# Optimization experiments

Hardware: AMD Instinct MI355X
Metric: run time of the kernel (lower is better)

Reference implementation:

```python
import jax, jax.numpy as jnp
import numpy as np

B, T, P = 4, 512, 3584          # batch, new tokens per seq, cached tokens per seq
D_MODEL, H, KH, DH = 2048, 16, 4, 128
N_REP = H // KH
MAX_SEQ = 4096
ROPE_BASE = 1e6
EPS = 1e-6


def _rmsnorm(t, w):
    # t: [..., DH]
    var = jnp.mean(t * t, axis=-1, keepdims=True)
    return t * jax.lax.rsqrt(var + EPS) * w


def _rope(t, positions):
    # t: [N, heads, DH], positions: [N] int
    half = DH // 2
    inv_freq = (1.0 / ROPE_BASE) ** (2.0 * jnp.arange(half, dtype=jnp.float32) / DH)
    theta = positions.astype(jnp.float32)[:, None] * inv_freq[None, :]   # [N, half]
    theta = jnp.concatenate([theta, theta], axis=-1)                      # [N, DH]
    sin = jnp.sin(theta)[:, None, :]
    cos = jnp.cos(theta)[:, None, :]
    x1, x2 = jnp.split(t, 2, axis=-1)
    rot = jnp.concatenate([-x2, x1], axis=-1)
    return cos * t + sin * rot


def setup_inputs() -> dict:
    key = jax.random.key(0)
    ks = jax.random.split(key, 9)
    N = B * T
    x = jax.random.normal(ks[0], (N, D_MODEL), dtype=jnp.float32)
    k_cache = jax.random.normal(ks[1], (B, KH, P, DH), dtype=jnp.float32)
    v_cache = jax.random.normal(ks[2], (B, KH, P, DH), dtype=jnp.float32)
    s = 1.0 / np.sqrt(D_MODEL)
    w_q = jax.random.normal(ks[3], (H * DH, D_MODEL), dtype=jnp.float32) * s
    w_k = jax.random.normal(ks[4], (KH * DH, D_MODEL), dtype=jnp.float32) * s
    w_v = jax.random.normal(ks[5], (KH * DH, D_MODEL), dtype=jnp.float32) * s
    w_o = jax.random.normal(ks[6], (D_MODEL, H * DH), dtype=jnp.float32) * s
    q_norm_w = jnp.ones((DH,), dtype=jnp.float32)
    k_norm_w = jnp.ones((DH,), dtype=jnp.float32)
    # each sequence's new tokens occupy absolute positions [P, P+T)
    positions = jnp.tile(P + jnp.arange(T, dtype=jnp.int32), B)  # [B*T]
    return {"x": x, "k_cache": k_cache, "v_cache": v_cache,
            "w_q": w_q, "w_k": w_k, "w_v": w_v, "w_o": w_o,
            "q_norm_w": q_norm_w, "k_norm_w": k_norm_w,
            "positions": positions}


def reference(x, k_cache, v_cache, w_q, w_k, w_v, w_o, q_norm_w, k_norm_w, positions):
    N = x.shape[0]
    # QKV projections (no bias)
    q = (x @ w_q.T).reshape(N, H, DH)
    k = (x @ w_k.T).reshape(N, KH, DH)
    v = (x @ w_v.T).reshape(N, KH, DH)
    # per-head RMSNorm then RoPE at absolute positions
    q = _rope(_rmsnorm(q, q_norm_w), positions)
    k = _rope(_rmsnorm(k, k_norm_w), positions)
    # assemble full KV: cached (pre-rotated) past + new tokens
    k_new = k.reshape(B, T, KH, DH).transpose(0, 2, 1, 3)   # [B,KH,T,DH]
    v_new = v.reshape(B, T, KH, DH).transpose(0, 2, 1, 3)
    k_full = jnp.concatenate([k_cache, k_new], axis=2)       # [B,KH,P+T,DH]
    v_full = jnp.concatenate([v_cache, v_new], axis=2)
    # GQA: repeat each kv head n_rep times
    k_rep = jnp.repeat(k_full, N_REP, axis=1)                # [B,H,S,DH]
    v_rep = jnp.repeat(v_full, N_REP, axis=1)
    q4 = q.reshape(B, T, H, DH).transpose(0, 2, 1, 3)        # [B,H,T,DH]
    scale = 1.0 / jnp.sqrt(jnp.float32(DH))
    scores = jnp.einsum('bhtd,bhsd->bhts', q4, k_rep) * scale  # [B,H,T,P+T]
    # right-bottom causal mask: q_pos = P + t, kv_pos = s
    q_pos = P + jnp.arange(T)
    kv_pos = jnp.arange(P + T)
    mask = q_pos[:, None] >= kv_pos[None, :]
    scores = jnp.where(mask[None, None], scores, -jnp.inf)
    attn = jax.nn.softmax(scores, axis=-1)
    out = jnp.einsum('bhts,bhsd->bhtd', attn, v_rep)          # [B,H,T,DH]
    out = out.transpose(0, 2, 1, 3).reshape(N, H * DH)
    return out @ w_o.T
```

## Files before the change

kernel.cpp:

```cpp
#include <hip/hip_runtime.h>
#include <hip/hip_bf16.h>
#include <stdint.h>

#define B_   4
#define T_   512
#define P_   3584
#define S_   4096
#define H_   16
#define KH_  4
#define DM_  2048
#define DH_  128
#define NTOK 2048
#define NCHUNK 3
#define NROWS 32768

typedef __attribute__((ext_vector_type(8)))  short          bf16x8;
typedef __attribute__((ext_vector_type(4)))  float          f32x4;
typedef __attribute__((ext_vector_type(16))) float          f32x16;
typedef __attribute__((ext_vector_type(4)))  float          f4v;
typedef __attribute__((ext_vector_type(4)))  unsigned short us4v;

__device__ __forceinline__ unsigned short f2bf(float x) {
    union { float f; unsigned u; } v; v.f = x;
    unsigned r = v.u + 0x7FFFu + ((v.u >> 16) & 1u);
    return (unsigned short)(r >> 16);
}
__device__ __forceinline__ float bf2f(unsigned short b) {
    union { unsigned u; float f; } v; v.u = ((unsigned)b) << 16; return v.f;
}
__device__ __forceinline__ unsigned pkbf(float a, float b) {
    __hip_bfloat162 h = __float22bfloat162_rn(float2{a, b});
    union { __hip_bfloat162 h; unsigned u; } cv; cv.h = h; return cv.u;
}
__device__ __forceinline__ float ex2(float x) {
    float r; asm("v_exp_f32 %0, %1" : "=v"(r) : "v"(x)); return r;
}
__device__ __forceinline__ float max3f(float a, float b, float c) {
    float r; asm("v_max3_f32 %0, %1, %2, %3" : "=v"(r) : "v"(a), "v"(b), "v"(c)); return r;
}
__device__ __forceinline__ float sin_rev(float xf) {
    float r; asm("v_sin_f32 %0, %1" : "=v"(r) : "v"(xf)); return r;
}
__device__ __forceinline__ float cos_rev(float xf) {
    float r; asm("v_cos_f32 %0, %1" : "=v"(r) : "v"(xf)); return r;
}

#define GLDS16(gp, lp) __builtin_amdgcn_global_load_lds( \
    (const __attribute__((address_space(1))) void*)(gp), \
    (__attribute__((address_space(3))) void*)(lp), 16, 0, 0)

__global__ __launch_bounds__(256) void convert_all(
    const float* __restrict__ x,  const float* __restrict__ wq,
    const float* __restrict__ wk, const float* __restrict__ wv,
    const float* __restrict__ wo, const float* __restrict__ kc,
    const float* __restrict__ vc,
    unsigned short* __restrict__ xb,   unsigned short* __restrict__ wqkvb,
    unsigned short* __restrict__ wob,  unsigned short* __restrict__ kfull,
    unsigned short* __restrict__ vT)
{
    __shared__ unsigned short tile[64][65];
    if (blockIdx.x >= 2048) {
        const int id = blockIdx.x - 2048;
        const int bk = id / 112;
        const int rem = id % 112;
        const int st = rem >> 1;
        const int dt = rem & 1;
        const float* src = vc + ((size_t)bk * P_ + st * 64) * DH_ + dt * 64;
        const int tq = threadIdx.x & 15;
        const int ts = threadIdx.x >> 4;
        #pragma unroll
        for (int i = 0; i < 4; ++i) {
            const int si = ts + i * 16;
            f4v v = *(const f4v*)(src + (size_t)si * DH_ + tq * 4);
            tile[si][tq*4+0] = f2bf(v[0]); tile[si][tq*4+1] = f2bf(v[1]);
            tile[si][tq*4+2] = f2bf(v[2]); tile[si][tq*4+3] = f2bf(v[3]);
        }
        __syncthreads();
        unsigned short* dst = vT + ((size_t)bk * DH_ + dt * 64) * S_ + st * 64;
        const int sq = threadIdx.x & 15;
        const int td = threadIdx.x >> 4;
        #pragma unroll
        for (int i = 0; i < 4; ++i) {
            const int di = td + i * 16;
            us4v o;
            o[0] = tile[sq*4+0][di]; o[1] = tile[sq*4+1][di];
            o[2] = tile[sq*4+2][di]; o[3] = tile[sq*4+3][di];
            *(us4v*)(dst + (size_t)di * S_ + sq * 4) = o;
        }
        return;
    }
    const long total = 5505024;
    for (long i = (long)blockIdx.x * 256 + threadIdx.x; i < total;
         i += 2048L * 256) {
        const f4v* src; us4v* dst; long s4, d4;
        if (i < 1048576)      { src=(const f4v*)x;  dst=(us4v*)xb;              s4=i;         d4=s4; }
        else if (i < 2097152) { src=(const f4v*)wq; dst=(us4v*)wqkvb;           s4=i-1048576; d4=s4; }
        else if (i < 2359296) { src=(const f4v*)wk; dst=(us4v*)(wqkvb+4194304); s4=i-2097152; d4=s4; }
        else if (i < 2621440) { src=(const f4v*)wv; dst=(us4v*)(wqkvb+5242880); s4=i-2359296; d4=s4; }
        else if (i < 3670016) { src=(const f4v*)wo; dst=(us4v*)wob;             s4=i-2621440; d4=s4; }
        else                  { s4=i-3670016; long bk=s4/114688;
                                d4=bk*131072+(s4-bk*114688);
                                src=(const f4v*)kc; dst=(us4v*)kfull; }
        f4v v = src[s4];
        us4v o; o[0]=f2bf(v[0]); o[1]=f2bf(v[1]); o[2]=f2bf(v[2]); o[3]=f2bf(v[3]);
        dst[d4] = o;
    }
}

__global__ __launch_bounds__(256) void gemm_bt(
    const unsigned short* __restrict__ A, const unsigned short* __restrict__ Bw,
    void* __restrict__ C, int M, int N, int K, int obf16, int ksplit)
{
    __shared__ short As[2][128 * 32];
    __shared__ short Bs[2][128 * 32];
    const int tid = threadIdx.x, lane = tid & 63, w = tid >> 6;
    int bid = blockIdx.x, ks = 0;
    if (ksplit) { const int half = gridDim.x >> 1; ks = bid >= half; bid -= ks * half; }
    const int Ksl = ksplit ? (K >> 1) : K;
    const int k0base = ks * Ksl;
    const int nbn = N >> 7;
    const int cpx = nbn >> 3;
    const int xcd = bid & 7;
    const int rr = bid >> 3;
    const int bm = rr / cpx, bn = xcd * cpx + rr % cpx;
    const int m0 = bm << 7, n0 = bn << 7;
    const int wm = w >> 1, wn = w & 1;

    f32x4 acc[4][4];
    #pragma unroll
    for (int i = 0; i < 4; ++i)
        #pragma unroll
        for (int j = 0; j < 4; ++j)
            #pragma unroll
            for (int r = 0; r < 4; ++r) acc[i][j][r] = 0.f;

    const int arow = lane >> 2;
    const int acol = (lane & 3) << 3;

    auto stage = [&](int buf, int k0) {
        #pragma unroll
        for (int cc = 0; cc < 2; ++cc) {
            const int c = 2 * w + cc;
            GLDS16(A  + (size_t)(m0 + c * 16 + arow) * K + k0 + acol, &As[buf][c * 512]);
            GLDS16(Bw + (size_t)(n0 + c * 16 + arow) * K + k0 + acol, &Bs[buf][c * 512]);
        }
    };

    stage(0, k0base);
    __syncthreads();

    const int nk = Ksl >> 5;
    const int fr = lane & 15, fk = (lane >> 4) << 3;
    for (int t = 0; t < nk; ++t) {
        const int buf = t & 1;
        if (t + 1 < nk) stage(buf ^ 1, k0base + ((t + 1) << 5));
        bf16x8 a[4], b[4];
        #pragma unroll
        for (int i = 0; i < 4; ++i)
            a[i] = *(const bf16x8*)&As[buf][(wm * 64 + i * 16 + fr) * 32 + fk];
        #pragma unroll
        for (int j = 0; j < 4; ++j)
            b[j] = *(const bf16x8*)&Bs[buf][(wn * 64 + j * 16 + fr) * 32 + fk];
        __builtin_amdgcn_s_setprio(1);
        #pragma unroll
        for (int i = 0; i < 4; ++i)
            #pragma unroll
            for (int j = 0; j < 4; ++j)
                acc[i][j] = __builtin_amdgcn_mfma_f32_16x16x32_bf16(a[i], b[j], acc[i][j], 0, 0, 0);
        __builtin_amdgcn_s_setprio(0);
        __syncthreads();
    }

    const int er = lane >> 4, ec = lane & 15;
    const size_t cbase = (size_t)ks * M * N;
    #pragma unroll
    for (int i = 0; i < 4; ++i)
        #pragma unroll
        for (int j = 0; j < 4; ++j)
            #pragma unroll
            for (int r = 0; r < 4; ++r) {
                const int row = m0 + wm * 64 + i * 16 + er * 4 + r;
                const int col = n0 + wn * 64 + j * 16 + ec;
                if (obf16) ((unsigned short*)C)[cbase + (size_t)row * N + col] = f2bf(acc[i][j][r]);
                else       ((float*)C)[cbase + (size_t)row * N + col] = acc[i][j][r];
            }
}

__global__ __launch_bounds__(256) void reduce2(
    const float* __restrict__ p0, const float* __restrict__ p1,
    float* __restrict__ out)
{
    const int total4 = (DM_ * NTOK) / 4;
    for (int i = blockIdx.x * 256 + threadIdx.x; i < total4; i += 1024 * 256) {
        f4v a = ((const f4v*)p0)[i];
        f4v b = ((const f4v*)p1)[i];
        a[0] += b[0]; a[1] += b[1]; a[2] += b[2]; a[3] += b[3];
        ((f4v*)out)[i] = a;
    }
}

__global__ __launch_bounds__(256) void norm_rope(
    const unsigned short* __restrict__ qkv0, const unsigned short* __restrict__ qkv1,
    const float* __restrict__ qw, const float* __restrict__ kw,
    const int* __restrict__ pos,
    unsigned short* __restrict__ Qb, unsigned short* __restrict__ Kf,
    unsigned short* __restrict__ VT)
{
    const int task = blockIdx.x * 4 + (threadIdx.x >> 6);
    const int n = task / 24, idx = task % 24;
    const int lane = threadIdx.x & 63;
    const int b = n >> 9, t = n & 511;

    if (idx >= 20) {
        const int kh = idx - 20;
        const size_t off = (size_t)n * 3072 + 2560 + kh * 128;
        const unsigned short* s0_ = qkv0 + off;
        const unsigned short* s1_ = qkv1 + off;
        unsigned short* dstT = VT + (size_t)(b * KH_ + kh) * DH_ * S_ + (P_ + t);
        dstT[(size_t)lane * S_]        = f2bf(bf2f(s0_[lane]) + bf2f(s1_[lane]));
        dstT[(size_t)(lane + 64) * S_] = f2bf(bf2f(s0_[lane + 64]) + bf2f(s1_[lane + 64]));
        return;
    }
    const bool isq = idx < 16;
    const int hh = isq ? idx : (idx - 16);
    const size_t off = (size_t)n * 3072 + (isq ? hh * 128 : 2048 + hh * 128);
    const unsigned short* s0_ = qkv0 + off;
    const unsigned short* s1_ = qkv1 + off;
    const float* wn_ = isq ? qw : kw;
    float x0 = bf2f(s0_[lane]) + bf2f(s1_[lane]);
    float x1 = bf2f(s0_[lane + 64]) + bf2f(s1_[lane + 64]);
    float ss = x0 * x0 + x1 * x1;
    #pragma unroll
    for (int m = 1; m < 64; m <<= 1) ss += __shfl_xor(ss, m);
    const float rinv = rsqrtf(ss * (1.0f / 128.0f) + 1e-6f);
    float y0 = x0 * rinv * wn_[lane];
    float y1 = x1 * rinv * wn_[lane + 64];
    const float fr = ex2(-(float)lane * (19.931568569324174f / 64.0f));
    const float th = (float)pos[n] * fr;
    const float xr = th * 0.15915494309189535f;
    const float xf = xr - floorf(xr);
    const float sn = sin_rev(xf), cs = cos_rev(xf);
    float o0 = cs * y0 - sn * y1;
    float o1 = cs * y1 + sn * y0;
    unsigned short* dst;
    if (isq) {
        const float qs = 0.08838834764831845f * 1.4426950408889634f;
        o0 *= qs; o1 *= qs;
        dst = Qb + ((size_t)(b * H_ + hh) * T_ + t) * DH_;
    } else {
        dst = Kf + ((size_t)(b * KH_ + hh) * S_ + P_ + t) * DH_;
    }
    dst[lane]      = f2bf(o0);
    dst[lane + 64] = f2bf(o1);
}

__global__ __launch_bounds__(256, 3) void attn(
    const unsigned short* __restrict__ Qb, const unsigned short* __restrict__ Kf,
    const unsigned short* __restrict__ VT, unsigned short* __restrict__ op0,
    unsigned short* __restrict__ op1, unsigned short* __restrict__ op2,
    float2* __restrict__ ml)
{
    __shared__ short Ks[3][32 * 128];
    __shared__ short Vs[3][128 * 32];

    const int tid = threadIdx.x, lane = tid & 63, w = tid >> 6;
    const int c = blockIdx.x >> 8;
    const int y = blockIdx.x & 255;
    const int xcd = y & 7, slot = y >> 3;
    const int p = xcd + 8 * (slot >> 4);
    const int inner = slot & 15;
    const int b = p >> 2, kvh = p & 3;
    const int h = kvh * 4 + (inner >> 2);
    const int qt = inner & 3;
    const int t0 = qt * 128;

    const unsigned short* Qrow = Qb + (size_t)(b * H_ + h) * T_ * DH_;
    const unsigned short* Kb   = Kf + (size_t)(b * KH_ + kvh) * S_ * DH_;
    const unsigned short* VTb  = VT + (size_t)(b * KH_ + kvh) * DH_ * S_;

    const int ql = lane & 31;
    const int hi = lane >> 5;

    bf16x8 qf[8];
    {
        const unsigned short* qp = Qrow + (size_t)(t0 + w * 32 + ql) * DH_ + hi * 8;
        #pragma unroll
        for (int d0 = 0; d0 < 8; ++d0) qf[d0] = *(const bf16x8*)(qp + d0 * 16);
    }

    f32x16 o[4];
    #pragma unroll
    for (int d = 0; d < 4; ++d)
        #pragma unroll
        for (int r = 0; r < 16; ++r) o[d][r] = 0.f;
    float m_run = -INFINITY, l_run = 0.f;

    const int q_pos = P_ + t0 + w * 32 + ql;
    const int s_end_wave = P_ + t0 + w * 32 + 32;
    const int nt_full = (P_ + t0 + 128) >> 5;
    const int nj = (nt_full - c + 2) / 3;

    auto stage = [&](int buf, int tile) {
        const int s0 = tile << 5;
        #pragma unroll
        for (int cc = 0; cc < 2; ++cc) {
            const int cx = 2 * w + cc;
            const int krow = cx * 4 + (lane >> 4);
            const int kel  = 8 * ((lane & 15) ^ (krow & 15));
            GLDS16(Kb + (size_t)(s0 + krow) * DH_ + kel, &Ks[buf][cx * 512]);
            const int vrow = cx * 16 + (lane >> 2);
            const int vel  = 8 * ((lane & 3) ^ ((lane >> 3) & 3));
            GLDS16(VTb + (size_t)vrow * S_ + s0 + vel, &Vs[buf][cx * 512]);
        }
    };

    stage(0, c);
    if (nj > 1) stage(1, c + 3);

    for (int j = 0; j < nj; ++j) {
        if (j + 1 < nj) asm volatile("s_waitcnt vmcnt(4)" ::: "memory");
        else            asm volatile("s_waitcnt vmcnt(0)" ::: "memory");
        __builtin_amdgcn_s_barrier();
        if (j + 2 < nj) stage((j + 2) % 3, c + 3 * (j + 2));

        const int t = c + 3 * j;
        const int s0 = t << 5;
        const int buf = j % 3;
        if (s0 < s_end_wave) {
            f32x16 st;
            #pragma unroll
            for (int r = 0; r < 16; ++r) st[r] = 0.f;
            {
                const char* kbase = (const char*)&Ks[buf][0] + ql * 256;
                const int sw = 16 * (ql & 15);
                #pragma unroll
                for (int d0 = 0; d0 < 8; ++d0) {
                    bf16x8 kfr = *(const bf16x8*)(kbase + ((d0 * 32 + 16 * hi) ^ sw));
                    st = __builtin_amdgcn_mfma_f32_32x32x16_bf16(kfr, qf[d0], st, 0, 0, 0);
                }
            }
            if (s0 + 31 > P_ + t0 + w * 32) {
                #pragma unroll
                for (int r = 0; r < 16; ++r) {
                    const int srow = (r & 3) + 8 * (r >> 2) + 4 * hi;
                    if (s0 + srow > q_pos) st[r] = -INFINITY;
                }
            }
            float m0_ = max3f(st[0], st[1], st[2]),  m1_ = max3f(st[3], st[4], st[5]);
            float m2_ = max3f(st[6], st[7], st[8]),  m3_ = max3f(st[9], st[10], st[11]);
            float m4_ = max3f(st[12], st[13], st[14]);
            float pmax = fmaxf(max3f(m0_, m1_, m2_), max3f(m3_, m4_, st[15]));
            pmax = fmaxf(pmax, __shfl_xor(pmax, 32));
            if (!__all(pmax <= m_run + 11.5f)) {
                const float m_new = fmaxf(m_run, pmax);
                const float alpha = ex2(m_run - m_new);
                l_run *= alpha;
                #pragma unroll
                for (int r = 0; r < 16; ++r) {
                    const int qr = (r & 3) + 8 * (r >> 2) + 4 * hi;
                    const float a = __shfl(alpha, qr);
                    #pragma unroll
                    for (int d = 0; d < 4; ++d) o[d][r] *= a;
                }
                m_run = m_new;
            }
            float psum = 0.f;
            #pragma unroll
            for (int r = 0; r < 16; ++r) { st[r] = ex2(st[r] - m_run); psum += st[r]; }
            psum += __shfl_xor(psum, 32);
            l_run += psum;
            unsigned pk[8];
            #pragma unroll
            for (int u = 0; u < 8; ++u) pk[u] = pkbf(st[2 * u], st[2 * u + 1]);
            union { bf16x8 v; unsigned u[4]; } pa0, pa1;
            { unsigned xx = (unsigned)__shfl_xor((int)pk[2], 32); pa0.u[0] = hi ? xx : pk[0]; }
            { unsigned xx = (unsigned)__shfl_xor((int)pk[3], 32); pa0.u[1] = hi ? xx : pk[1]; }
            { unsigned xx = (unsigned)__shfl_xor((int)pk[0], 32); pa0.u[2] = hi ? pk[2] : xx; }
            { unsigned xx = (unsigned)__shfl_xor((int)pk[1], 32); pa0.u[3] = hi ? pk[3] : xx; }
            { unsigned xx = (unsigned)__shfl_xor((int)pk[6], 32); pa1.u[0] = hi ? xx : pk[4]; }
            { unsigned xx = (unsigned)__shfl_xor((int)pk[7], 32); pa1.u[1] = hi ? xx : pk[5]; }
            { unsigned xx = (unsigned)__shfl_xor((int)pk[4], 32); pa1.u[2] = hi ? pk[6] : xx; }
            { unsigned xx = (unsigned)__shfl_xor((int)pk[5], 32); pa1.u[3] = hi ? pk[7] : xx; }
            #pragma unroll
            for (int ch = 0; ch < 2; ++ch)
                #pragma unroll
                for (int db = 0; db < 4; ++db) {
                    const int vrow = db * 32 + ql;
                    bf16x8 vf = *(const bf16x8*)&Vs[buf][vrow * 32 + 8 * ((2 * ch + hi) ^ ((ql >> 1) & 3))];
                    o[db] = __builtin_amdgcn_mfma_f32_32x32x16_bf16(
                        ch ? pa1.v : pa0.v, vf, o[db], 0, 0, 0);
                }
        }
    }

    unsigned short* op = (c == 0) ? op0 : (c == 1) ? op1 : op2;
    const int rowbase = (b * H_ + h) * T_ + t0 + w * 32;
    if (hi == 0) ml[c * NROWS + rowbase + ql] = float2{m_run, l_run};
    #pragma unroll
    for (int r = 0; r < 16; ++r) {
        const int qr = (r & 3) + 8 * (r >> 2) + 4 * hi;
        unsigned short* orow = op + (size_t)(rowbase + qr) * DH_;
        #pragma unroll
        for (int d = 0; d < 4; ++d)
            orow[d * 32 + ql] = f2bf(o[d][r]);
    }
}

__global__ __launch_bounds__(256) void combine(
    const float2* __restrict__ ml,
    const unsigned short* __restrict__ op0, const unsigned short* __restrict__ op1,
    const unsigned short* __restrict__ op2, unsigned short* __restrict__ ao)
{
    const int row = blockIdx.x * 4 + (threadIdx.x >> 6);
    const int lane = threadIdx.x & 63;
    const float2 a0 = ml[row], a1 = ml[NROWS + row], a2 = ml[2 * NROWS + row];
    const float m = fmaxf(a0.x, fmaxf(a1.x, a2.x));
    const float w0 = ex2(a0.x - m), w1 = ex2(a1.x - m), w2 = ex2(a2.x - m);
    const float Linv = 1.0f / (w0 * a0.y + w1 * a1.y + w2 * a2.y);
    const size_t src = (size_t)row * DH_ + 2 * lane;
    const unsigned u0 = *(const unsigned*)(op0 + src);
    const unsigned u1 = *(const unsigned*)(op1 + src);
    const unsigned u2 = *(const unsigned*)(op2 + src);
    const float v0 = (bf2f((unsigned short)u0) * w0 + bf2f((unsigned short)u1) * w1 +
                      bf2f((unsigned short)u2) * w2) * Linv;
    const float v1 = (bf2f((unsigned short)(u0 >> 16)) * w0 + bf2f((unsigned short)(u1 >> 16)) * w1 +
                      bf2f((unsigned short)(u2 >> 16)) * w2) * Linv;
    const int t = row & 511, h = (row >> 9) & 15, b = row >> 13;
    unsigned short* dst = ao + ((size_t)(b * T_ + t) * (H_ * DH_)) + h * DH_ + 2 * lane;
    *(unsigned*)dst = pkbf(v0, v1);
}

extern "C" void kernel_launch(void* const* d_in, const int* in_sizes, int n_in,
                              void* d_out, int out_size, void* d_ws, size_t ws_size,
                              hipStream_t stream)
{
    const float* x   = (const float*)d_in[0];
    const float* kc  = (const float*)d_in[1];
    const float* vc  = (const float*)d_in[2];
    const float* wq  = (const float*)d_in[3];
    const float* wk  = (const float*)d_in[4];
    const float* wv  = (const float*)d_in[5];
    const float* wo  = (const float*)d_in[6];
    const float* qnw = (const float*)d_in[7];
    const float* knw = (const float*)d_in[8];
    const int*   pos = (const int*)d_in[9];
    float* out = (float*)d_out;

    char* ws = (char*)d_ws;
    unsigned short* xb    = (unsigned short*)(ws + 0);
    unsigned short* wqkvb = (unsigned short*)(ws + 8388608);
    unsigned short* wob   = (unsigned short*)(ws + 20971520);
    unsigned short* qkvp0 = (unsigned short*)(ws + 29360128);
    unsigned short* qkvp1 = (unsigned short*)(ws + 41943040);
    unsigned short* qb    = (unsigned short*)(ws + 54525952);
    unsigned short* kfull = (unsigned short*)(ws + 62914560);
    unsigned short* vT    = (unsigned short*)(ws + 79691776);
    unsigned short* op0   = (unsigned short*)(ws + 0);
    unsigned short* op1   = (unsigned short*)(ws + 8388608);
    float2*         ml    = (float2*)(ws + 16777216);
    unsigned short* op2   = (unsigned short*)(ws + 29360128);
    unsigned short* ao    = (unsigned short*)(ws + 37748736);
    float*          po0   = (float*)(ws + 62914560);

    hipLaunchKernelGGL(convert_all, dim3(2048 + 1792), dim3(256), 0, stream,
                       x, wq, wk, wv, wo, kc, vc, xb, wqkvb, wob, kfull, vT);
    hipLaunchKernelGGL(gemm_bt, dim3(2 * 16 * 24), dim3(256), 0, stream,
                       xb, wqkvb, (void*)qkvp0, 2048, 3072, 2048, 1, 1);
    hipLaunchKernelGGL(norm_rope, dim3(NTOK * 24 / 4), dim3(256), 0, stream,
                       qkvp0, qkvp1, qnw, knw, pos, qb, kfull, vT);
    hipLaunchKernelGGL(attn, dim3(NCHUNK * 256), dim3(256), 0, stream,
                       qb, kfull, vT, op0, op1, op2, ml);
    hipLaunchKernelGGL(combine, dim3(NROWS / 4), dim3(256), 0, stream,
                       ml, op0, op1, op2, ao);
    hipLaunchKernelGGL(gemm_bt, dim3(2 * 16 * 16), dim3(256), 0, stream,
                       ao, wob, (void*)po0, 2048, 2048, 2048, 0, 1);
    hipLaunchKernelGGL(reduce2, dim3(1024), dim3(256), 0, stream,
                       po0, po0 + (size_t)DM_ * NTOK, out);
}
```

Measured before the change: 217.1 us.

## Software-pipeline QK^T of the next KV tile with softmax and PV of the current one

The attention loop now computes the QK^T MFMAs for tile j+1 before doing the masking, online softmax and PV MFMAs for tile j, so the two matrix phases can overlap with the softmax arithmetic. LDS staging grows from three to four K/V buffers to keep one tile loading while two are in use. The wait and barrier move to sit just before the next tile's QK^T. Launch bounds drop from three to two blocks per CU to make room for the extra score accumulator registers, which reduces occupancy. The GEMM k-split flag becomes a split count, but it is still called with 2, so that part behaves the same as before.

Result: slower. 235.7 us (+8.6%).

```diff
diff --git a/kernel.cpp b/kernel.cpp
--- a/kernel.cpp
+++ b/kernel.cpp
@@ -109,14 +109,16 @@
 
 __global__ __launch_bounds__(256) void gemm_bt(
     const unsigned short* __restrict__ A, const unsigned short* __restrict__ Bw,
-    void* __restrict__ C, int M, int N, int K, int obf16, int ksplit)
+    void* __restrict__ C, int M, int N, int K, int obf16, int nks)
 {
     __shared__ short As[2][128 * 32];
     __shared__ short Bs[2][128 * 32];
     const int tid = threadIdx.x, lane = tid & 63, w = tid >> 6;
-    int bid = blockIdx.x, ks = 0;
-    if (ksplit) { const int half = gridDim.x >> 1; ks = bid >= half; bid -= ks * half; }
-    const int Ksl = ksplit ? (K >> 1) : K;
+    int bid = blockIdx.x;
+    const int bps = gridDim.x / nks;
+    const int ks = bid / bps;
+    bid -= ks * bps;
+    const int Ksl = K / nks;
     const int k0base = ks * Ksl;
     const int nbn = N >> 7;
     const int cpx = nbn >> 3;
@@ -254,14 +256,14 @@
     dst[lane + 64] = f2bf(o1);
 }
 
-__global__ __launch_bounds__(256, 3) void attn(
+__global__ __launch_bounds__(256, 2) void attn(
     const unsigned short* __restrict__ Qb, const unsigned short* __restrict__ Kf,
     const unsigned short* __restrict__ VT, unsigned short* __restrict__ op0,
     unsigned short* __restrict__ op1, unsigned short* __restrict__ op2,
     float2* __restrict__ ml)
 {
-    __shared__ short Ks[3][32 * 128];
-    __shared__ short Vs[3][128 * 32];
+    __shared__ short Ks[4][32 * 128];
+    __shared__ short Vs[4][128 * 32];
 
     const int tid = threadIdx.x, lane = tid & 63, w = tid >> 6;
     const int c = blockIdx.x >> 8;
@@ -314,31 +316,44 @@
         }
     };
 
+    auto qk = [&](int tile, int buf, f32x16& stv) {
+        #pragma unroll
+        for (int r = 0; r < 16; ++r) stv[r] = 0.f;
+        if ((tile << 5) < s_end_wave) {
+            const char* kbase = (const char*)&Ks[buf][0] + ql * 256;
+            const int sw = 16 * (ql & 15);
+            #pragma unroll
+            for (int d0 = 0; d0 < 8; ++d0) {
+                bf16x8 kfr = *(const bf16x8*)(kbase + ((d0 * 32 + 16 * hi) ^ sw));
+                stv = __builtin_amdgcn_mfma_f32_32x32x16_bf16(kfr, qf[d0], stv, 0, 0, 0);
+            }
+        }
+    };
+
     stage(0, c);
-    if (nj > 1) stage(1, c + 3);
+    if (nj > 1) {
+        stage(1, c + 3);
+        asm volatile("s_waitcnt vmcnt(4)" ::: "memory");
+    } else {
+        asm volatile("s_waitcnt vmcnt(0)" ::: "memory");
+    }
+    __builtin_amdgcn_s_barrier();
+    f32x16 st;
+    qk(c, 0, st);
 
     for (int j = 0; j < nj; ++j) {
-        if (j + 1 < nj) asm volatile("s_waitcnt vmcnt(4)" ::: "memory");
-        else            asm volatile("s_waitcnt vmcnt(0)" ::: "memory");
-        __builtin_amdgcn_s_barrier();
-        if (j + 2 < nj) stage((j + 2) % 3, c + 3 * (j + 2));
-
+        if (j + 2 < nj) stage((j + 2) & 3, c + 3 * (j + 2));
+        f32x16 st2;
+        if (j + 1 < nj) {
+            if (j + 2 < nj) asm volatile("s_waitcnt vmcnt(4)" ::: "memory");
+            else            asm volatile("s_waitcnt vmcnt(0)" ::: "memory");
+            __builtin_amdgcn_s_barrier();
+            qk(c + 3 * (j + 1), (j + 1) & 3, st2);
+        }
         const int t = c + 3 * j;
         const int s0 = t << 5;
-        const int buf = j % 3;
+        const int buf = j & 3;
         if (s0 < s_end_wave) {
-            f32x16 st;
-            #pragma unroll
-            for (int r = 0; r < 16; ++r) st[r] = 0.f;
-            {
-                const char* kbase = (const char*)&Ks[buf][0] + ql * 256;
-                const int sw = 16 * (ql & 15);
-                #pragma unroll
-                for (int d0 = 0; d0 < 8; ++d0) {
-                    bf16x8 kfr = *(const bf16x8*)(kbase + ((d0 * 32 + 16 * hi) ^ sw));
-                    st = __builtin_amdgcn_mfma_f32_32x32x16_bf16(kfr, qf[d0], st, 0, 0, 0);
-                }
-            }
             if (s0 + 31 > P_ + t0 + w * 32) {
                 #pragma unroll
                 for (int r = 0; r < 16; ++r) {
@@ -391,6 +406,7 @@
                         ch ? pa1.v : pa0.v, vf, o[db], 0, 0, 0);
                 }
         }
+        st = st2;
     }
 
     unsigned short* op = (c == 0) ? op0 : (c == 1) ? op1 : op2;
@@ -465,7 +481,7 @@
     hipLaunchKernelGGL(convert_all, dim3(2048 + 1792), dim3(256), 0, stream,
                        x, wq, wk, wv, wo, kc, vc, xb, wqkvb, wob, kfull, vT);
     hipLaunchKernelGGL(gemm_bt, dim3(2 * 16 * 24), dim3(256), 0, stream,
-                       xb, wqkvb, (void*)qkvp0, 2048, 3072, 2048, 1, 1);
+                       xb, wqkvb, (void*)qkvp0, 2048, 3072, 2048, 1, 2);
     hipLaunchKernelGGL(norm_rope, dim3(NTOK * 24 / 4), dim3(256), 0, stream,
                        qkvp0, qkvp1, qnw, knw, pos, qb, kfull, vT);
     hipLaunchKernelGGL(attn, dim3(NCHUNK * 256), dim3(256), 0, stream,
@@ -473,7 +489,7 @@
     hipLaunchKernelGGL(combine, dim3(NROWS / 4), dim3(256), 0, stream,
                        ml, op0, op1, op2, ao);
     hipLaunchKernelGGL(gemm_bt, dim3(2 * 16 * 16), dim3(256), 0, stream,
-                       ao, wob, (void*)po0, 2048, 2048, 2048, 0, 1);
+                       ao, wob, (void*)po0, 2048, 2048, 2048, 0, 2);
     hipLaunchKernelGGL(reduce2, dim3(1024), dim3(256), 0, stream,
                        po0, po0 + (size_t)DM_ * NTOK, out);
 }
```
